# Optimization experiments

Hardware: AMD Instinct MI355X
Metric: run time of the kernel (lower is better)

The kernel has to match this reference:

```python
import jax, jax.numpy as jnp
import numpy as np

EMBED_DIM = 128
HIDDEN_DIM = 32
BN_EPS = 1e-5


def setup_inputs() -> dict:
    key = jax.random.key(0)
    ks = jax.random.split(key, 11)
    B, N, D, H = 16, 2048, EMBED_DIM, HIDDEN_DIM
    s_d = 1.0 / np.sqrt(D)
    return {
        "f_in": jax.random.normal(ks[0], (B, N, D), dtype=jnp.float32),
        "w_q": jax.random.uniform(ks[1], (H, D), jnp.float32, -s_d, s_d),
        "b_q": jax.random.uniform(ks[2], (H,), jnp.float32, -s_d, s_d),
        "w_k": jax.random.uniform(ks[3], (H, D), jnp.float32, -s_d, s_d),
        "b_k": jax.random.uniform(ks[4], (H,), jnp.float32, -s_d, s_d),
        "w_v": jax.random.uniform(ks[5], (D, D), jnp.float32, -s_d, s_d),
        "b_v": jax.random.uniform(ks[6], (D,), jnp.float32, -s_d, s_d),
        "w_l": jax.random.uniform(ks[7], (D, D), jnp.float32, -s_d, s_d),
        "b_l": jax.random.uniform(ks[8], (D,), jnp.float32, -s_d, s_d),
        "bn_gamma": jnp.ones((D,), jnp.float32),
        "bn_beta": jnp.zeros((D,), jnp.float32),
    }


def reference(f_in, w_q, b_q, w_k, b_k, w_v, b_v, w_l, b_l, bn_gamma, bn_beta):
    # Q/K/V projections: (B, N, D) -> (B, N, h) / (B, N, D)
    q = jnp.einsum("bnd,hd->bnh", f_in, w_q) + b_q
    k = jnp.einsum("bnd,hd->bnh", f_in, w_k) + b_k
    v = jnp.einsum("bnd,ed->bne", f_in, w_v) + b_v
    # scores (B, N, N); softmax over dim=1 (query axis), then L1-renorm over keys
    a = jnp.einsum("bnh,bmh->bnm", q, k)
    a = jax.nn.softmax(a, axis=1)
    a = a / jnp.sum(a, axis=2, keepdims=True)
    f_sa = jnp.einsum("bnm,bme->bne", a, v)
    # LBR: Linear -> BatchNorm (training stats over B and N) -> ReLU, residual add
    x = f_in - f_sa
    y = jnp.einsum("bnd,ed->bne", x, w_l) + b_l
    mean = jnp.mean(y, axis=(0, 1))
    var = jnp.var(y, axis=(0, 1))  # biased, as BatchNorm uses for normalization
    y = bn_gamma * (y - mean) * jax.lax.rsqrt(var + BN_EPS) + bn_beta
    return jax.nn.relu(y) + f_sa
```

## Files before the change

### kernel.cpp

```cpp
#include <hip/hip_runtime.h>
#include <stdint.h>

#define NB 16
#define NN 2048
#define ND 128
#define NH 32
#define NS (NB*NN)

typedef __attribute__((ext_vector_type(8))) short bf16x8;
typedef __attribute__((ext_vector_type(4))) float f32x4;
typedef __attribute__((ext_vector_type(16))) float f32x16;
typedef __attribute__((ext_vector_type(2))) int i32x2;

__device__ __forceinline__ unsigned short f2bf(float f){
  union { float f; unsigned int u; } v; v.f = f;
  unsigned int r = v.u + 0x7fffu + ((v.u >> 16) & 1u);
  return (unsigned short)(r >> 16);
}
__device__ __forceinline__ float bf2f(unsigned short u){
  union { unsigned int u; float f; } v; v.u = ((unsigned int)u) << 16;
  return v.f;
}
__device__ __forceinline__ float fexp2(float x){
  float r; asm("v_exp_f32 %0, %1" : "=v"(r) : "v"(x)); return r;
}
__device__ __forceinline__ void pswap(unsigned int &x, unsigned int &y){
#if __has_builtin(__builtin_amdgcn_permlane32_swap)
  i32x2 r = __builtin_amdgcn_permlane32_swap((int)x, (int)y, false, false);
  x = (unsigned int)r[0]; y = (unsigned int)r[1];
#else
  unsigned int sx = (unsigned int)__shfl_xor((int)x, 32, 64);
  unsigned int sy = (unsigned int)__shfl_xor((int)y, 32, 64);
  bool hi = ((threadIdx.x & 63) >> 5) != 0;
  unsigned int nx = hi ? sy : x;
  unsigned int ny = hi ? y  : sx;
  x = nx; y = ny;
#endif
}

__global__ __launch_bounds__(256) void k_prep(const float* wq, const float* wk, const float* wv, const float* wl,
                                              unsigned short* oq, unsigned short* ok, unsigned short* ov, unsigned short* ol){
  int i = blockIdx.x*256 + threadIdx.x;
  if (i < 4096) oq[i] = f2bf(wq[i]);
  else if (i < 8192) ok[i-4096] = f2bf(wk[i-4096]);
  else if (i < 24576) ov[i-8192] = f2bf(wv[i-8192]);
  else if (i < 40960) ol[i-24576] = f2bf(wl[i-24576]);
}

__global__ __launch_bounds__(256) void k_qkv(const float* f, const unsigned short* wbq, const unsigned short* wbk,
                                             const unsigned short* wbv, const float* bq, const float* bk, const float* bv,
                                             unsigned short* Qb, unsigned short* Kb, unsigned short* Vb){
  int tid = threadIdx.x, wave = tid>>6, lane = tid&63, lr = lane&15, lg = lane>>4;
  long r0 = (long)blockIdx.x*64 + wave*16;
  bf16x8 a[4];
  const float* frow = f + (r0 + lr)*ND;
  #pragma unroll
  for (int ks=0; ks<4; ks++){
    const float* p = frow + ks*32 + lg*8;
    bf16x8 t;
    #pragma unroll
    for (int j=0;j<8;j++) t[j] = (short)f2bf(p[j]);
    a[ks] = t;
  }
  #pragma unroll
  for (int cs=0; cs<12; cs++){
    const unsigned short* wsrc; const float* bsrc; int cl;
    if (cs<2){ wsrc=wbq; bsrc=bq; cl=cs*16; }
    else if (cs<4){ wsrc=wbk; bsrc=bk; cl=(cs-2)*16; }
    else { wsrc=wbv; bsrc=bv; cl=(cs-4)*16; }
    f32x4 acc = {0.f,0.f,0.f,0.f};
    #pragma unroll
    for (int ks=0;ks<4;ks++){
      bf16x8 b = *(const bf16x8*)(wsrc + (cl+lr)*ND + ks*32 + lg*8);
      acc = __builtin_amdgcn_mfma_f32_16x16x32_bf16(a[ks], b, acc, 0, 0, 0);
    }
    float bias = bsrc[cl + lr];
    #pragma unroll
    for (int r=0;r<4;r++){
      float v = acc[r] + bias;
      if (cs<2) v *= 1.4426950408889634f;
      long row = r0 + lg*4 + r;
      if (cs<2) Qb[row*NH + cl+lr] = f2bf(v);
      else if (cs<4) Kb[row*NH + cl+lr] = f2bf(v);
      else Vb[row*ND + cl+lr] = f2bf(v);
    }
  }
}

__global__ __launch_bounds__(256) void k_csv(const unsigned short* Qb, const unsigned short* Kb,
                                             const unsigned short* Vb, unsigned short* VT){
  __shared__ unsigned short tr[128][65];
  __shared__ float wsh[64];
  int tid=threadIdx.x, wave=tid>>6, lane=tid&63, lr=lane&15, lg=lane>>4;
  int wg = (blockIdx.x & 7)*64 + (blockIdx.x >> 3);
  int b = wg >> 5;
  int m0 = (wg & 31)*64;
  const unsigned short* Qbb = Qb + (long)b*NN*NH;
  const unsigned short* Kbb = Kb + (long)b*NN*NH;
  const unsigned short* Vbb = Vb + ((long)b*NN + m0)*ND;
  bf16x8 vreg[4];
  #pragma unroll
  for (int it=0; it<4; it++){
    int i = it*256 + tid;
    int r = i >> 4, c8 = (i & 15)*8;
    vreg[it] = *(const bf16x8*)(Vbb + r*ND + c8);
  }
  bf16x8 kf = *(const bf16x8*)(Kbb + (m0 + wave*16 + lr)*NH + lg*8);
  float csum = 0.f;
  for (int n0=0; n0<NN; n0+=64){
    #pragma unroll
    for (int u=0; u<4; u++){
      bf16x8 qf = *(const bf16x8*)(Qbb + (n0+u*16+lr)*NH + lg*8);
      f32x4 c = {0.f,0.f,0.f,0.f};
      c = __builtin_amdgcn_mfma_f32_16x16x32_bf16(qf, kf, c, 0, 0, 0);
      csum += fexp2(c[0]) + fexp2(c[1]) + fexp2(c[2]) + fexp2(c[3]);
    }
  }
  csum += __shfl_xor(csum, 16, 64);
  csum += __shfl_xor(csum, 32, 64);
  #pragma unroll
  for (int it=0; it<4; it++){
    int i = it*256 + tid;
    int r = i >> 4, c8 = (i & 15)*8;
    #pragma unroll
    for (int j=0;j<8;j++) tr[c8+j][r] = (unsigned short)vreg[it][j];
  }
  if (lg == 0) wsh[wave*16 + lr] = 1.f / csum;
  __syncthreads();
  unsigned short* VTb = VT + (long)b*160*NN;
  #pragma unroll
  for (int it=0; it<9; it++){
    int i = it*256 + tid;
    int e = i >> 4, m4 = (i & 15)*4;
    ushort4 o;
    if (e < 128){
      o.x = f2bf(bf2f(tr[e][m4+0]) * wsh[m4+0]);
      o.y = f2bf(bf2f(tr[e][m4+1]) * wsh[m4+1]);
      o.z = f2bf(bf2f(tr[e][m4+2]) * wsh[m4+2]);
      o.w = f2bf(bf2f(tr[e][m4+3]) * wsh[m4+3]);
    } else if (e == 128){
      o.x = f2bf(wsh[m4+0]); o.y = f2bf(wsh[m4+1]);
      o.z = f2bf(wsh[m4+2]); o.w = f2bf(wsh[m4+3]);
    } else { o.x = o.y = o.z = o.w = 0; }
    *(ushort4*)(VTb + (long)e*NN + m0 + m4) = o;
  }
  {
    int e = 144 + (tid >> 4), m4 = (tid & 15)*4;
    ushort4 z; z.x = z.y = z.z = z.w = 0;
    *(ushort4*)(VTb + (long)e*NN + m0 + m4) = z;
  }
}

__global__ __launch_bounds__(256) void k_pv(const unsigned short* Qb, const unsigned short* Kb,
                                            const unsigned short* VT, unsigned short* pnum, float* pden){
  __shared__ __align__(16) unsigned char vts[3][20480];
  int tid=threadIdx.x, wave=tid>>6, lane=tid&63;
  int l31 = lane & 31, H = lane >> 5;
  int wg = (blockIdx.x & 7)*64 + (blockIdx.x >> 3);
  int half = wg & 1;
  int bq = wg >> 1;
  int b = bq >> 4;
  int q0 = (bq & 15)*128 + wave*32;
  int mbase = half*1024;
  const int NT2 = 16;
  const unsigned short* Qbb = Qb + (long)b*NN*NH;
  const unsigned short* Kbb = Kb + (long)b*NN*NH;
  const unsigned short* VTb = VT + (long)b*160*NN;

  auto stageV = [&](int buf, int m0c){
    #pragma unroll
    for (int t=0;t<5;t++){
      int i = wave*5 + t;
      int e = i*8 + (lane>>3);
      int sblk = (lane&7) ^ (e&7);
      __builtin_amdgcn_global_load_lds(
        (const __attribute__((address_space(1))) unsigned int*)(VTb + (long)e*NN + m0c + sblk*8),
        (__attribute__((address_space(3))) unsigned int*)(&vts[buf][i*1024]), 16, 0, 0);
    }
  };

  bf16x8 qf0 = *(const bf16x8*)(Qbb + (long)(q0 + l31)*NH + 8*H);
  bf16x8 qf1 = *(const bf16x8*)(Qbb + (long)(q0 + l31)*NH + 16 + 8*H);
  bf16x8 k00 = *(const bf16x8*)(Kbb + (long)(mbase + l31)*NH + 8*H);
  bf16x8 k01 = *(const bf16x8*)(Kbb + (long)(mbase + l31)*NH + 16 + 8*H);
  bf16x8 k10 = *(const bf16x8*)(Kbb + (long)(mbase + 32 + l31)*NH + 8*H);
  bf16x8 k11 = *(const bf16x8*)(Kbb + (long)(mbase + 32 + l31)*NH + 16 + 8*H);
  asm volatile("" ::: "memory");
  stageV(0, mbase);
  asm volatile("" ::: "memory");
  stageV(1, mbase + 64);
  asm volatile("" ::: "memory");

  f32x16 acc[5];
  #pragma unroll
  for (int c=0;c<5;c++)
    #pragma unroll
    for (int r=0;r<16;r++) acc[c][r] = 0.f;

  union U { unsigned int u[4]; bf16x8 v; };

  int vc = 0, vs = 2;
  for (int it = 0; it < NT2; ++it){
    if (it == 0)        asm volatile("s_waitcnt vmcnt(5)" ::: "memory");
    else if (it < NT2-1) asm volatile("s_waitcnt vmcnt(9)" ::: "memory");
    else                asm volatile("s_waitcnt vmcnt(0)" ::: "memory");
    __builtin_amdgcn_s_barrier();
    bf16x8 n00, n01, n10, n11;
    bool pf = (it + 1 < NT2);
    if (pf){
      long mb = mbase + (long)(it+1)*64;
      n00 = *(const bf16x8*)(Kbb + (mb + l31)*NH + 8*H);
      n01 = *(const bf16x8*)(Kbb + (mb + l31)*NH + 16 + 8*H);
      n10 = *(const bf16x8*)(Kbb + (mb + 32 + l31)*NH + 8*H);
      n11 = *(const bf16x8*)(Kbb + (mb + 32 + l31)*NH + 16 + 8*H);
    }
    asm volatile("" ::: "memory");
    if (it + 2 < NT2) stageV(vs, mbase + (it+2)*64);
    asm volatile("" ::: "memory");
    const unsigned char* vcur = &vts[vc][0];

    #pragma unroll
    for (int t=0;t<2;t++){
      f32x16 s;
      #pragma unroll
      for (int r=0;r<16;r++) s[r] = 0.f;
      s = __builtin_amdgcn_mfma_f32_32x32x16_bf16(t ? k10 : k00, qf0, s, 0, 0, 0);
      s = __builtin_amdgcn_mfma_f32_32x32x16_bf16(t ? k11 : k01, qf1, s, 0, 0, 0);
      #pragma unroll
      for (int r=0;r<16;r++) s[r] = fexp2(s[r]);
      unsigned int pk[8];
      #pragma unroll
      for (int p=0;p<8;p++)
        asm("v_cvt_pk_bf16_f32 %0, %1, %2" : "=v"(pk[p]) : "v"(s[2*p]), "v"(s[2*p+1]));
      pswap(pk[0], pk[2]);
      pswap(pk[1], pk[3]);
      pswap(pk[4], pk[6]);
      pswap(pk[5], pk[7]);
      U fa0, fa1;
      fa0.u[0] = pk[0]; fa0.u[1] = pk[1]; fa0.u[2] = pk[2]; fa0.u[3] = pk[3];
      fa1.u[0] = pk[4]; fa1.u[1] = pk[5]; fa1.u[2] = pk[6]; fa1.u[3] = pk[7];
      __builtin_amdgcn_s_setprio(1);
      #pragma unroll
      for (int ksl=0; ksl<2; ksl++){
        int KS = 2*t + ksl;
        const U& fa = ksl ? fa1 : fa0;
        #pragma unroll
        for (int c=0;c<5;c++){
          int e = c*32 + l31;
          bf16x8 vb = *(const bf16x8*)(vcur + (e<<7) + (((2*KS + H) ^ (e&7))<<4));
          acc[c] = __builtin_amdgcn_mfma_f32_32x32x16_bf16(fa.v, vb, acc[c], 0, 0, 0);
        }
      }
      __builtin_amdgcn_s_setprio(0);
    }
    if (pf){ k00 = n00; k01 = n01; k10 = n10; k11 = n11; }
    vc = (vc==2)?0:vc+1;
    vs = (vs==2)?0:vs+1;
  }
  unsigned short* pn = pnum + (long)half*NS*ND + (long)b*NN*ND;
  float* pd = pden + (long)half*NS + (long)b*NN;
  #pragma unroll
  for (int r=0;r<16;r++){
    int rho = (r&3) + 8*(r>>2) + 4*H;
    long q = q0 + rho;
    #pragma unroll
    for (int c=0;c<4;c++)
      pn[q*ND + c*32 + l31] = f2bf(acc[c][r]);
    if (l31 == 0) pd[q] = acc[4][r];
  }
}

__global__ __launch_bounds__(256) void k_comb(const unsigned short* pnum, const float* pden, unsigned short* fsab){
  long i0 = ((long)blockIdx.x*256 + threadIdx.x)*8;
  long q = i0 >> 7;
  float rinv = 1.f / (pden[q] + pden[NS + q]);
  bf16x8 a = *(const bf16x8*)(pnum + i0);
  bf16x8 bb = *(const bf16x8*)(pnum + (long)NS*ND + i0);
  bf16x8 o;
  #pragma unroll
  for (int j=0;j<8;j++)
    o[j] = (short)f2bf((bf2f((unsigned short)a[j]) + bf2f((unsigned short)bb[j])) * rinv);
  *(bf16x8*)(fsab + i0) = o;
}

__global__ __launch_bounds__(256) void k_lin(const float* f, const unsigned short* fsab, const unsigned short* wbl, const float* bl,
                                             unsigned short* ybuf, float* part){
  __shared__ float psum[4][128], psq[4][128];
  int tid=threadIdx.x, wave=tid>>6, lane=tid&63, lr=lane&15, lg=lane>>4;
  long r0 = (long)blockIdx.x*64 + wave*16;
  bf16x8 a[4];
  {
    const float* fr = f + (r0+lr)*ND;
    const unsigned short* sr = fsab + (r0+lr)*ND;
    #pragma unroll
    for (int ks=0;ks<4;ks++){
      bf16x8 sv = *(const bf16x8*)(sr + ks*32 + lg*8);
      bf16x8 t;
      #pragma unroll
      for (int j=0;j<8;j++){
        int d = ks*32 + lg*8 + j;
        t[j] = (short)f2bf(fr[d] - bf2f((unsigned short)sv[j]));
      }
      a[ks] = t;
    }
  }
  #pragma unroll
  for (int cs=0;cs<8;cs++){
    f32x4 acc = {0.f,0.f,0.f,0.f};
    #pragma unroll
    for (int ks=0;ks<4;ks++){
      bf16x8 bfr = *(const bf16x8*)(wbl + (cs*16+lr)*ND + ks*32 + lg*8);
      acc = __builtin_amdgcn_mfma_f32_16x16x32_bf16(a[ks], bfr, acc, 0, 0, 0);
    }
    float bias = bl[cs*16+lr];
    float l1=0.f, l2=0.f;
    #pragma unroll
    for (int r=0;r<4;r++){
      float y = acc[r] + bias;
      ybuf[(r0 + lg*4 + r)*ND + cs*16 + lr] = f2bf(y);
      l1 += y; l2 += y*y;
    }
    l1 += __shfl_xor(l1,16,64); l1 += __shfl_xor(l1,32,64);
    l2 += __shfl_xor(l2,16,64); l2 += __shfl_xor(l2,32,64);
    if (lg==0){ psum[wave][cs*16+lr] = l1; psq[wave][cs*16+lr] = l2; }
  }
  __syncthreads();
  if (tid < 128){
    float t1 = psum[0][tid]+psum[1][tid]+psum[2][tid]+psum[3][tid];
    float t2 = psq[0][tid]+psq[1][tid]+psq[2][tid]+psq[3][tid];
    part[tid*512 + blockIdx.x] = t1;
    part[65536 + tid*512 + blockIdx.x] = t2;
  }
}

__global__ __launch_bounds__(64) void k_bnred(const float* part, const float* gamma, const float* beta, float* bnstat){
  int c = blockIdx.x, t = threadIdx.x;
  float s=0.f, q=0.f;
  for (int i=t; i<512; i+=64){ s += part[c*512+i]; q += part[65536 + c*512+i]; }
  #pragma unroll
  for (int m=1; m<64; m<<=1){ s += __shfl_xor(s,m,64); q += __shfl_xor(q,m,64); }
  if (t==0){
    float mean = s * (1.f/(float)NS);
    float var  = q * (1.f/(float)NS) - mean*mean;
    float rstd = rsqrtf(var + 1e-5f);
    float sc = gamma[c]*rstd;
    bnstat[c] = sc;
    bnstat[128+c] = beta[c] - mean*sc;
  }
}

__global__ __launch_bounds__(256) void k_final(const unsigned short* ybuf, const unsigned short* fsab, const float* bnstat,
                                               float* out){
  long i0 = ((long)blockIdx.x*256 + threadIdx.x)*8;
  int c0 = (int)(i0 & (ND-1));
  bf16x8 yv = *(const bf16x8*)(ybuf + i0);
  bf16x8 fv = *(const bf16x8*)(fsab + i0);
  f32x4 o0, o1;
  #pragma unroll
  for (int j=0;j<8;j++){
    int c = c0 + j;
    float v = bf2f((unsigned short)yv[j]) * bnstat[c] + bnstat[128+c];
    v = v > 0.f ? v : 0.f;
    float r = v + bf2f((unsigned short)fv[j]);
    if (j<4) o0[j] = r; else o1[j-4] = r;
  }
  *(f32x4*)(out + i0) = o0;
  *(f32x4*)(out + i0 + 4) = o1;
}

extern "C" void kernel_launch(void* const* d_in, const int* in_sizes, int n_in,
                              void* d_out, int out_size, void* d_ws, size_t ws_size,
                              hipStream_t stream){
  const float* f_in  = (const float*)d_in[0];
  const float* w_q   = (const float*)d_in[1];
  const float* b_q   = (const float*)d_in[2];
  const float* w_k   = (const float*)d_in[3];
  const float* b_k   = (const float*)d_in[4];
  const float* w_v   = (const float*)d_in[5];
  const float* b_v   = (const float*)d_in[6];
  const float* w_l   = (const float*)d_in[7];
  const float* b_l   = (const float*)d_in[8];
  const float* gamma = (const float*)d_in[9];
  const float* beta  = (const float*)d_in[10];
  float* out = (float*)d_out;
  char* ws = (char*)d_ws;

  unsigned short* wbq = (unsigned short*)(ws + 0);
  unsigned short* wbk = (unsigned short*)(ws + 8192);
  unsigned short* wbv = (unsigned short*)(ws + 16384);
  unsigned short* wbl = (unsigned short*)(ws + 49152);
  unsigned short* Qb  = (unsigned short*)(ws + 81920);
  unsigned short* Kb  = (unsigned short*)(ws + 2179072);
  unsigned short* VT  = (unsigned short*)(ws + 4276224);
  unsigned short* Vb  = (unsigned short*)(ws + 14761984);
  unsigned short* fsab= (unsigned short*)(ws + 14761984);
  unsigned short* pnum= (unsigned short*)(ws + 23150592);
  unsigned short* ybuf= (unsigned short*)(ws + 23150592);
  float*          part= (float*)(ws + 31539200);
  float*          pden= (float*)(ws + 39927808);
  float*          bnst= (float*)(ws + 40189952);

  k_prep  <<<160, 256, 0, stream>>>(w_q, w_k, w_v, w_l, wbq, wbk, wbv, wbl);
  k_qkv   <<<512, 256, 0, stream>>>(f_in, wbq, wbk, wbv, b_q, b_k, b_v, Qb, Kb, Vb);
  k_csv   <<<512, 256, 0, stream>>>(Qb, Kb, Vb, VT);
  k_pv    <<<512, 256, 0, stream>>>(Qb, Kb, VT, pnum, pden);
  k_comb  <<<2048,256, 0, stream>>>(pnum, pden, fsab);
  k_lin   <<<512, 256, 0, stream>>>(f_in, fsab, wbl, b_l, ybuf, part);
  k_bnred <<<128, 64, 0, stream>>>(part, gamma, beta, bnst);
  k_final <<<2048,256, 0, stream>>>(ybuf, fsab, bnst, out);
}
```

Before: 115.9 us.

## Software-pipeline score/exp ahead of PV MFMAs and fuse combine into linear kernel

The attention kernel is restructured so the score MFMA and exp for the next key tile are computed after the current tile's PV MFMAs. The loop is unrolled by two with ping-pong packed-probability buffers, which lets the score and exp work overlap with the PV matrix ops and the outstanding loads. Separately, the k_comb kernel is removed and its normalize-and-sum of the two partial numerators is folded into k_lin, which also writes fsab. This saves one launch and a full read and write pass over pnum. Workspace aliases for ybuf and part are moved to free regions. The costs are higher register pressure from the extra buffers and a loop that assumes an even NT2.

After: 114.7 us. About the same (-1.1%).

```diff
diff --git a/kernel.cpp b/kernel.cpp
--- a/kernel.cpp
+++ b/kernel.cpp
@@ -181,15 +181,6 @@
 
   bf16x8 qf0 = *(const bf16x8*)(Qbb + (long)(q0 + l31)*NH + 8*H);
   bf16x8 qf1 = *(const bf16x8*)(Qbb + (long)(q0 + l31)*NH + 16 + 8*H);
-  bf16x8 k00 = *(const bf16x8*)(Kbb + (long)(mbase + l31)*NH + 8*H);
-  bf16x8 k01 = *(const bf16x8*)(Kbb + (long)(mbase + l31)*NH + 16 + 8*H);
-  bf16x8 k10 = *(const bf16x8*)(Kbb + (long)(mbase + 32 + l31)*NH + 8*H);
-  bf16x8 k11 = *(const bf16x8*)(Kbb + (long)(mbase + 32 + l31)*NH + 16 + 8*H);
-  asm volatile("" ::: "memory");
-  stageV(0, mbase);
-  asm volatile("" ::: "memory");
-  stageV(1, mbase + 64);
-  asm volatile("" ::: "memory");
 
   f32x16 acc[5];
   #pragma unroll
@@ -199,33 +190,14 @@
 
   union U { unsigned int u[4]; bf16x8 v; };
 
-  int vc = 0, vs = 2;
-  for (int it = 0; it < NT2; ++it){
-    if (it == 0)        asm volatile("s_waitcnt vmcnt(5)" ::: "memory");
-    else if (it < NT2-1) asm volatile("s_waitcnt vmcnt(9)" ::: "memory");
-    else                asm volatile("s_waitcnt vmcnt(0)" ::: "memory");
-    __builtin_amdgcn_s_barrier();
-    bf16x8 n00, n01, n10, n11;
-    bool pf = (it + 1 < NT2);
-    if (pf){
-      long mb = mbase + (long)(it+1)*64;
-      n00 = *(const bf16x8*)(Kbb + (mb + l31)*NH + 8*H);
-      n01 = *(const bf16x8*)(Kbb + (mb + l31)*NH + 16 + 8*H);
-      n10 = *(const bf16x8*)(Kbb + (mb + 32 + l31)*NH + 8*H);
-      n11 = *(const bf16x8*)(Kbb + (mb + 32 + l31)*NH + 16 + 8*H);
-    }
-    asm volatile("" ::: "memory");
-    if (it + 2 < NT2) stageV(vs, mbase + (it+2)*64);
-    asm volatile("" ::: "memory");
-    const unsigned char* vcur = &vts[vc][0];
-
+  auto SCORE = [&](bf16x8 a0, bf16x8 a1, bf16x8 b0, bf16x8 b1, unsigned int* w){
     #pragma unroll
     for (int t=0;t<2;t++){
       f32x16 s;
       #pragma unroll
       for (int r=0;r<16;r++) s[r] = 0.f;
-      s = __builtin_amdgcn_mfma_f32_32x32x16_bf16(t ? k10 : k00, qf0, s, 0, 0, 0);
-      s = __builtin_amdgcn_mfma_f32_32x32x16_bf16(t ? k11 : k01, qf1, s, 0, 0, 0);
+      s = __builtin_amdgcn_mfma_f32_32x32x16_bf16(t ? b0 : a0, qf0, s, 0, 0, 0);
+      s = __builtin_amdgcn_mfma_f32_32x32x16_bf16(t ? b1 : a1, qf1, s, 0, 0, 0);
       #pragma unroll
       for (int r=0;r<16;r++) s[r] = fexp2(s[r]);
       unsigned int pk[8];
@@ -236,14 +208,21 @@
       pswap(pk[1], pk[3]);
       pswap(pk[4], pk[6]);
       pswap(pk[5], pk[7]);
-      U fa0, fa1;
-      fa0.u[0] = pk[0]; fa0.u[1] = pk[1]; fa0.u[2] = pk[2]; fa0.u[3] = pk[3];
-      fa1.u[0] = pk[4]; fa1.u[1] = pk[5]; fa1.u[2] = pk[6]; fa1.u[3] = pk[7];
-      __builtin_amdgcn_s_setprio(1);
+      #pragma unroll
+      for (int j=0;j<8;j++) w[t*8+j] = pk[j];
+    }
+  };
+
+  auto PV = [&](const unsigned int* w, const unsigned char* vcur){
+    __builtin_amdgcn_s_setprio(1);
+    #pragma unroll
+    for (int t=0;t<2;t++){
       #pragma unroll
       for (int ksl=0; ksl<2; ksl++){
         int KS = 2*t + ksl;
-        const U& fa = ksl ? fa1 : fa0;
+        U fa;
+        #pragma unroll
+        for (int i2=0;i2<4;i2++) fa.u[i2] = w[t*8 + ksl*4 + i2];
         #pragma unroll
         for (int c=0;c<5;c++){
           int e = c*32 + l31;
@@ -251,12 +230,53 @@
           acc[c] = __builtin_amdgcn_mfma_f32_32x32x16_bf16(fa.v, vb, acc[c], 0, 0, 0);
         }
       }
-      __builtin_amdgcn_s_setprio(0);
-    }
-    if (pf){ k00 = n00; k01 = n01; k10 = n10; k11 = n11; }
+    }
+    __builtin_amdgcn_s_setprio(0);
+  };
+
+  stageV(0, mbase);
+  stageV(1, mbase + 64);
+  asm volatile("" ::: "memory");
+  bf16x8 k00 = *(const bf16x8*)(Kbb + (long)(mbase + l31)*NH + 8*H);
+  bf16x8 k01 = *(const bf16x8*)(Kbb + (long)(mbase + l31)*NH + 16 + 8*H);
+  bf16x8 k10 = *(const bf16x8*)(Kbb + (long)(mbase + 32 + l31)*NH + 8*H);
+  bf16x8 k11 = *(const bf16x8*)(Kbb + (long)(mbase + 32 + l31)*NH + 16 + 8*H);
+  asm volatile("s_waitcnt vmcnt(0)" ::: "memory");
+  unsigned int eA[16], eB[16];
+  SCORE(k00, k01, k10, k11, eA);
+
+  int vc = 0, vs = 2;
+  auto BODY = [&](int it, unsigned int* Ein, unsigned int* Eout){
+    __builtin_amdgcn_s_barrier();
+    asm volatile("" ::: "memory");
+    bool pf = (it + 1 < NT2);
+    bf16x8 n00, n01, n10, n11;
+    if (pf){
+      long mb = mbase + (long)(it+1)*64;
+      n00 = *(const bf16x8*)(Kbb + (mb + l31)*NH + 8*H);
+      n01 = *(const bf16x8*)(Kbb + (mb + l31)*NH + 16 + 8*H);
+      n10 = *(const bf16x8*)(Kbb + (mb + 32 + l31)*NH + 8*H);
+      n11 = *(const bf16x8*)(Kbb + (mb + 32 + l31)*NH + 16 + 8*H);
+    }
+    asm volatile("" ::: "memory");
+    if (it + 2 < NT2) stageV(vs, mbase + (it+2)*64);
+    asm volatile("" ::: "memory");
+    PV(Ein, &vts[vc][0]);
+    if (pf){
+      if (it + 2 < NT2) asm volatile("s_waitcnt vmcnt(5)" ::: "memory");
+      else              asm volatile("s_waitcnt vmcnt(0)" ::: "memory");
+      __builtin_amdgcn_sched_barrier(0);
+      SCORE(n00, n01, n10, n11, Eout);
+    }
     vc = (vc==2)?0:vc+1;
     vs = (vs==2)?0:vs+1;
-  }
+  };
+
+  for (int it2 = 0; it2 < NT2; it2 += 2){
+    BODY(it2,   eA, eB);
+    BODY(it2+1, eB, eA);
+  }
+
   unsigned short* pn = pnum + (long)half*NS*ND + (long)b*NN*ND;
   float* pd = pden + (long)half*NS + (long)b*NN;
   #pragma unroll
@@ -270,38 +290,33 @@
   }
 }
 
-__global__ __launch_bounds__(256) void k_comb(const unsigned short* pnum, const float* pden, unsigned short* fsab){
-  long i0 = ((long)blockIdx.x*256 + threadIdx.x)*8;
-  long q = i0 >> 7;
-  float rinv = 1.f / (pden[q] + pden[NS + q]);
-  bf16x8 a = *(const bf16x8*)(pnum + i0);
-  bf16x8 bb = *(const bf16x8*)(pnum + (long)NS*ND + i0);
-  bf16x8 o;
-  #pragma unroll
-  for (int j=0;j<8;j++)
-    o[j] = (short)f2bf((bf2f((unsigned short)a[j]) + bf2f((unsigned short)bb[j])) * rinv);
-  *(bf16x8*)(fsab + i0) = o;
-}
-
-__global__ __launch_bounds__(256) void k_lin(const float* f, const unsigned short* fsab, const unsigned short* wbl, const float* bl,
-                                             unsigned short* ybuf, float* part){
+__global__ __launch_bounds__(256) void k_lin(const float* f, const unsigned short* pnum, const float* pden,
+                                             const unsigned short* wbl, const float* bl,
+                                             unsigned short* fsab, unsigned short* ybuf, float* part){
   __shared__ float psum[4][128], psq[4][128];
   int tid=threadIdx.x, wave=tid>>6, lane=tid&63, lr=lane&15, lg=lane>>4;
   long r0 = (long)blockIdx.x*64 + wave*16;
+  long row = r0 + lr;
+  float rinv = 1.f / (pden[row] + pden[NS + row]);
   bf16x8 a[4];
   {
-    const float* fr = f + (r0+lr)*ND;
-    const unsigned short* sr = fsab + (r0+lr)*ND;
+    const float* fr = f + row*ND;
+    const unsigned short* p0 = pnum + row*ND;
+    const unsigned short* p1 = pnum + (long)NS*ND + row*ND;
     #pragma unroll
     for (int ks=0;ks<4;ks++){
-      bf16x8 sv = *(const bf16x8*)(sr + ks*32 + lg*8);
-      bf16x8 t;
+      bf16x8 v0 = *(const bf16x8*)(p0 + ks*32 + lg*8);
+      bf16x8 v1 = *(const bf16x8*)(p1 + ks*32 + lg*8);
+      bf16x8 t, fs;
       #pragma unroll
       for (int j=0;j<8;j++){
         int d = ks*32 + lg*8 + j;
-        t[j] = (short)f2bf(fr[d] - bf2f((unsigned short)sv[j]));
+        float sa = (bf2f((unsigned short)v0[j]) + bf2f((unsigned short)v1[j])) * rinv;
+        fs[j] = (short)f2bf(sa);
+        t[j] = (short)f2bf(fr[d] - bf2f((unsigned short)fs[j]));
       }
       a[ks] = t;
+      *(bf16x8*)(fsab + row*ND + ks*32 + lg*8) = fs;
     }
   }
   #pragma unroll
@@ -390,13 +405,13 @@
   unsigned short* wbv = (unsigned short*)(ws + 16384);
   unsigned short* wbl = (unsigned short*)(ws + 49152);
   unsigned short* Qb  = (unsigned short*)(ws + 81920);
+  float*          part= (float*)(ws + 81920);
   unsigned short* Kb  = (unsigned short*)(ws + 2179072);
   unsigned short* VT  = (unsigned short*)(ws + 4276224);
+  unsigned short* ybuf= (unsigned short*)(ws + 4276224);
   unsigned short* Vb  = (unsigned short*)(ws + 14761984);
   unsigned short* fsab= (unsigned short*)(ws + 14761984);
   unsigned short* pnum= (unsigned short*)(ws + 23150592);
-  unsigned short* ybuf= (unsigned short*)(ws + 23150592);
-  float*          part= (float*)(ws + 31539200);
   float*          pden= (float*)(ws + 39927808);
   float*          bnst= (float*)(ws + 40189952);
 
@@ -404,8 +419,7 @@
   k_qkv   <<<512, 256, 0, stream>>>(f_in, wbq, wbk, wbv, b_q, b_k, b_v, Qb, Kb, Vb);
   k_csv   <<<512, 256, 0, stream>>>(Qb, Kb, Vb, VT);
   k_pv    <<<512, 256, 0, stream>>>(Qb, Kb, VT, pnum, pden);
-  k_comb  <<<2048,256, 0, stream>>>(pnum, pden, fsab);
-  k_lin   <<<512, 256, 0, stream>>>(f_in, fsab, wbl, b_l, ybuf, part);
+  k_lin   <<<512, 256, 0, stream>>>(f_in, pnum, pden, wbl, b_l, fsab, ybuf, part);
   k_bnred <<<128, 64, 0, stream>>>(part, gamma, beta, bnst);
   k_final <<<2048,256, 0, stream>>>(ybuf, fsab, bnst, out);
 }
```
